# Kernel tuning notes

Hardware: AMD Instinct MI355X
Metric: run time of the kernel (lower is better)

The kernel has to match this reference:

```python
import jax, jax.numpy as jnp
import numpy as np

DIM = 1024
N_HEADS = 16
HEAD_DIM = DIM // N_HEADS
B, T = 2, 2048


def setup_inputs() -> dict:
    key = jax.random.key(0)
    ks = jax.random.split(key, 5)
    x = jax.random.normal(ks[0], (B, T, DIM), dtype=jnp.float32)
    s = DIM ** -0.5
    Wq = jax.random.normal(ks[1], (DIM, DIM), dtype=jnp.float32) * s
    Wk = jax.random.normal(ks[2], (DIM, DIM), dtype=jnp.float32) * s
    Wv = jax.random.normal(ks[3], (DIM, DIM), dtype=jnp.float32) * s
    Wo = jax.random.normal(ks[4], (DIM, DIM), dtype=jnp.float32) * s
    # causal mask: 1 where attendable, 0 where masked (masked_fill on mask==0)
    mask = jnp.tril(jnp.ones((T, T), dtype=jnp.int32))[None, None, :, :]
    return {"x": x, "Wq": Wq, "Wk": Wk, "Wv": Wv, "Wo": Wo, "mask": mask}


def _rope_tables(seq_len, dim, dtype):
    inv_freq = 1.0 / (10000.0 ** (jnp.arange(0, dim, 2, dtype=jnp.float32) / dim))
    t = jnp.arange(seq_len, dtype=jnp.float32)
    freqs = jnp.outer(t, inv_freq)               # [T, dim/2]
    emb = jnp.concatenate([freqs, freqs], -1)    # [T, dim]
    return jnp.cos(emb).astype(dtype), jnp.sin(emb).astype(dtype)


def _rotate_half(t):
    h = t.shape[-1] // 2
    return jnp.concatenate([-t[..., h:], t[..., :h]], axis=-1)


def reference(x, Wq, Wk, Wv, Wo, mask):
    Bq, Tq, C = x.shape
    H, Dh = N_HEADS, C // N_HEADS
    q = (x @ Wq.T).reshape(Bq, Tq, H, Dh)
    k = (x @ Wk.T).reshape(Bq, Tq, H, Dh)
    v = (x @ Wv.T).reshape(Bq, Tq, H, Dh)
    cos, sin = _rope_tables(Tq, Dh, x.dtype)
    cos = cos[None, :, None, :]   # [1,T,1,Dh]
    sin = sin[None, :, None, :]
    q = q * cos + _rotate_half(q) * sin
    k = k * cos + _rotate_half(k) * sin
    scale = Dh ** -0.5
    # [B,H,T,T]
    attn = jnp.einsum('bqhd,bkhd->bhqk', q, k) * scale
    attn = jnp.where(mask == 0, jnp.float32(-jnp.inf).astype(attn.dtype), attn)
    attn = jax.nn.softmax(attn, axis=-1)
    out = jnp.einsum('bhqk,bkhd->bqhd', attn, v).reshape(Bq, Tq, C)
    return out @ Wo.T
```

## Files before the change

### kernel.cpp

```cpp
#include <hip/hip_runtime.h>
#include <stdint.h>


typedef float  f32x4  __attribute__((ext_vector_type(4)));
typedef float  f32x16 __attribute__((ext_vector_type(16)));
typedef __bf16 bf16x8 __attribute__((ext_vector_type(8)));
typedef unsigned int u32x2 __attribute__((ext_vector_type(2)));

#define GLDS16(gp, lp)                                                         \
  __builtin_amdgcn_global_load_lds(                                            \
      (const __attribute__((address_space(1))) void*)(gp),                     \
      (__attribute__((address_space(3))) void*)(lp), 16, 0, 0)

static __device__ __forceinline__ f32x4 zero4() {
  f32x4 z = {0.f, 0.f, 0.f, 0.f};
  return z;
}

static __device__ __forceinline__ bf16x8 cvt8(const float* __restrict__ p) {
  f32x4 u = *(const f32x4*)p;
  f32x4 v = *(const f32x4*)(p + 4);
  bf16x8 o;
#pragma unroll
  for (int j = 0; j < 4; ++j) o[j] = (__bf16)u[j];
#pragma unroll
  for (int j = 0; j < 4; ++j) o[4 + j] = (__bf16)v[j];
  return o;
}

__global__ __launch_bounds__(256) void prep(
    const float* __restrict__ x,
    const float* __restrict__ Wq, const float* __restrict__ Wk,
    const float* __restrict__ Wv, const float* __restrict__ Wo,
    __bf16* __restrict__ xb, __bf16* __restrict__ Wb)
{
  size_t g = ((size_t)blockIdx.x * 256 + threadIdx.x) * 8;
  if (g < (size_t)4194304) {
    *(bf16x8*)&xb[g] = cvt8(x + g);
  } else {
    size_t j = g - 4194304;
    int w = (int)(j >> 20);
    size_t off = j & 1048575;
    const float* src = (w == 0) ? Wq : (w == 1) ? Wk : (w == 2) ? Wv : Wo;
    *(bf16x8*)&Wb[(size_t)w * 1048576 + off] = cvt8(src + off);
  }
}

__global__ __launch_bounds__(256) void gemm_qkv(
    const __bf16* __restrict__ xb, const __bf16* __restrict__ Wb,
    __bf16* __restrict__ Qp, __bf16* __restrict__ Kp, __bf16* __restrict__ Vt)
{
  __shared__ __bf16 Smem[2 * 128 * 64];
  __bf16* As = Smem;
  __bf16* Bs = Smem + 128 * 64;

  const int tid  = threadIdx.x;
  const int lane = tid & 63;
  const int wid  = tid >> 6;
  const int quad = lane >> 4;
  const int l16  = lane & 15;
  const int wm   = (wid >> 1) * 64;
  const int wn   = (wid & 1) * 64;

  const int lin = blockIdx.x;
  const int n0  = (lin & 7) * 128;
  const int r2  = lin >> 3;
  const int z   = r2 % 3;
  const int m0  = (r2 / 3) * 128;
  const __bf16* Bt = Wb + (size_t)z * 1048576;

  const int sr  = tid >> 3;
  const int scx = ((tid & 7) ^ (sr & 7)) * 8;
  const int fx  = l16 & 7;

  f32x4 acc[4][4];
  for (int i = 0; i < 4; ++i)
    for (int j = 0; j < 4; ++j) acc[i][j] = zero4();

  for (int k0 = 0; k0 < 1024; k0 += 64) {
    __syncthreads();
#pragma unroll
    for (int c = 0; c < 4; ++c) {
      GLDS16(xb + (size_t)(m0 + c * 32 + sr) * 1024 + k0 + scx,
             &As[c * 2048 + (size_t)tid * 8]);
      GLDS16(Bt + (size_t)(n0 + c * 32 + sr) * 1024 + k0 + scx,
             &Bs[c * 2048 + (size_t)tid * 8]);
    }
    __syncthreads();

#pragma unroll
    for (int ks = 0; ks < 2; ++ks) {
      bf16x8 af[4], bfr[4];
#pragma unroll
      for (int i = 0; i < 4; ++i)
        af[i] = *(const bf16x8*)
            &As[(wm + i * 16 + l16) * 64 + ((ks * 4 + quad) ^ fx) * 8];
#pragma unroll
      for (int i = 0; i < 4; ++i)
        bfr[i] = *(const bf16x8*)
            &Bs[(wn + i * 16 + l16) * 64 + ((ks * 4 + quad) ^ fx) * 8];
#pragma unroll
      for (int mt = 0; mt < 4; ++mt)
#pragma unroll
        for (int nt = 0; nt < 4; ++nt)
          acc[mt][nt] = __builtin_amdgcn_mfma_f32_16x16x32_bf16(
              af[mt], bfr[nt], acc[mt][nt], 0, 0, 0);
    }
  }

  __syncthreads();

  const int h = (n0 + wn) >> 6;
  __bf16* es = &Smem[wid * 1152];
  const int rl = lane >> 3, ch = lane & 7;

  if (z < 2) {
    const float c0f = -13.287712379549449f / 32.0f;
    const float f0 = exp2f((float)l16 * c0f);
    const float f1 = exp2f((float)(16 + l16) * c0f);
    const float SC = (z == 0) ? 0.125f * 1.44269504088896340736f : 1.0f;
    for (int mt = 0; mt < 4; ++mt)
      for (int r = 0; r < 4; ++r) {
        int gm = m0 + wm + mt * 16 + 4 * quad + r;
        float tt = (float)(gm & 2047);
        for (int nt = 0; nt < 2; ++nt) {
          float ang = tt * (nt ? f1 : f0);
          float cv = __cosf(ang) * SC, sv = __sinf(ang) * SC;
          float lo = acc[mt][nt][r], hi = acc[mt][nt + 2][r];
          acc[mt][nt][r]     = lo * cv - hi * sv;
          acc[mt][nt + 2][r] = hi * cv + lo * sv;
        }
      }
    __bf16* dst = (z == 0) ? Qp : Kp;
    for (int mt = 0; mt < 4; ++mt) {
      for (int nt = 0; nt < 4; ++nt)
        for (int r = 0; r < 4; ++r)
          es[(4 * quad + r) * 72 + nt * 16 + l16] = (__bf16)acc[mt][nt][r];
      size_t g0 = (size_t)(m0 + wm + mt * 16 + rl) * 1024 + n0 + wn + ch * 8;
      *(bf16x8*)&dst[g0]            = *(const bf16x8*)&es[rl * 72 + ch * 8];
      *(bf16x8*)&dst[g0 + 8 * 1024] = *(const bf16x8*)&es[(rl + 8) * 72 + ch * 8];
    }
  } else {
    const int b = m0 >> 11;
    const size_t hb = (size_t)(b * 16 + h) * 64;
    const int tt = (m0 + wm) & 2047;
    for (int nt = 0; nt < 4; ++nt) {
      for (int mt = 0; mt < 4; ++mt)
        for (int r = 0; r < 4; ++r)
          es[l16 * 72 + mt * 16 + 4 * quad + r] = (__bf16)acc[mt][nt][r];
      size_t g0 = (hb + nt * 16 + rl) * 2048 + tt + ch * 8;
      *(bf16x8*)&Vt[g0]                     = *(const bf16x8*)&es[rl * 72 + ch * 8];
      *(bf16x8*)&Vt[g0 + (size_t)8 * 2048]  = *(const bf16x8*)&es[(rl + 8) * 72 + ch * 8];
    }
  }
}

__global__ __launch_bounds__(256) void attn_fwd(
    __bf16* QA, const __bf16* __restrict__ Kp,
    const __bf16* __restrict__ Vt)
{
  __shared__ __bf16 Ks[2][64 * 64];
  __shared__ __bf16 Vs[2][64 * 64];

  const int tid  = threadIdx.x;
  const int lane = tid & 63, wid = tid >> 6;
  const int hl = lane >> 5, lq = lane & 31, lq7 = lq & 7;
  const int qh = wid & 1, kh = wid >> 1;

  const int L  = blockIdx.x;
  const int j  = L >> 3;
  const int qb = 31 - (j >> 2);
  const int bh = (L & 7) * 4 + (j & 3);
  const int b = bh >> 4, h = bh & 15;
  const int q0 = qb * 64;

  const size_t rowb = (size_t)b * 2048;
  const __bf16* Vb = Vt + (size_t)bh * 64 * 2048;

  const int srow = lane >> 3;
  const int scol = ((lane & 7) ^ srow) * 8;
  const int ck0 = wid * 2, ck1 = wid * 2 + 1;

  const int iql = qh * 32 + lq;

  bf16x8 qa[4];
#pragma unroll
  for (int ks = 0; ks < 4; ++ks)
    qa[ks] = *(const bf16x8*)
        &QA[(rowb + q0 + iql) * 1024 + h * 64 + ks * 16 + hl * 8];

  f32x16 oacc[2];
#pragma unroll
  for (int dt = 0; dt < 2; ++dt)
#pragma unroll
    for (int r = 0; r < 16; ++r) oacc[dt][r] = 0.f;
  float l_i = 0.f;

  const int kcmax = qb;

  GLDS16(Kp + (rowb + ck0 * 8 + srow) * 1024 + h * 64 + scol, &Ks[0][ck0 * 512]);
  GLDS16(Kp + (rowb + ck1 * 8 + srow) * 1024 + h * 64 + scol, &Ks[0][ck1 * 512]);
  GLDS16(Vb + (size_t)(ck0 * 8 + srow) * 2048 + scol, &Vs[0][ck0 * 512]);
  GLDS16(Vb + (size_t)(ck1 * 8 + srow) * 2048 + scol, &Vs[0][ck1 * 512]);
  __syncthreads();

  for (int kc = 0; kc <= kcmax; ++kc) {
    const int c = kc & 1;
    if (kc < kcmax) {
      const int t0 = (kc + 1) * 64;
      GLDS16(Kp + (rowb + t0 + ck0 * 8 + srow) * 1024 + h * 64 + scol,
             &Ks[c ^ 1][ck0 * 512]);
      GLDS16(Kp + (rowb + t0 + ck1 * 8 + srow) * 1024 + h * 64 + scol,
             &Ks[c ^ 1][ck1 * 512]);
      GLDS16(Vb + (size_t)(ck0 * 8 + srow) * 2048 + t0 + scol,
             &Vs[c ^ 1][ck0 * 512]);
      GLDS16(Vb + (size_t)(ck1 * 8 + srow) * 2048 + t0 + scol,
             &Vs[c ^ 1][ck1 * 512]);
    }

    const __bf16* Ksb = Ks[c];
    const __bf16* Vsb = Vs[c];

    f32x16 sacc;
#pragma unroll
    for (int r = 0; r < 16; ++r) sacc[r] = -16.f;
    __builtin_amdgcn_s_setprio(1);
#pragma unroll
    for (int ks = 0; ks < 4; ++ks) {
      bf16x8 kf = *(const bf16x8*)
          &Ksb[(kh * 32 + lq) * 64 + (((2 * ks + hl) ^ lq7) * 8)];
      sacc = __builtin_amdgcn_mfma_f32_32x32x16_bf16(kf, qa[ks], sacc, 0, 0, 0);
    }
    __builtin_amdgcn_s_setprio(0);

    const bool diag = (kc == kcmax);
    float p[16];
    float rsum = 0.f;
#pragma unroll
    for (int r = 0; r < 16; ++r) {
      float s = sacc[r];
      if (diag) {
        int kp = kh * 32 + (r & 3) + 8 * (r >> 2) + 4 * hl;
        if (kp > iql) s = -1e30f;
      }
      p[r] = __builtin_amdgcn_exp2f(s);
      rsum += p[r];
    }
    rsum += __shfl_xor(rsum, 32, 64);
    l_i += rsum;

    unsigned int cpk[8];
#pragma unroll
    for (int i = 0; i < 8; ++i)
      asm("v_cvt_pk_bf16_f32 %0, %1, %2"
          : "=v"(cpk[i]) : "v"(p[2 * i]), "v"(p[2 * i + 1]));
    bf16x8 pb[2];
#pragma unroll
    for (int k2 = 0; k2 < 2; ++k2) {
      unsigned int a0 = cpk[4 * k2 + 0], b0 = cpk[4 * k2 + 2];
      unsigned int a1 = cpk[4 * k2 + 1], b1 = cpk[4 * k2 + 3];
      asm("v_permlane32_swap_b32 %0, %1" : "+v"(a0), "+v"(b0));
      asm("v_permlane32_swap_b32 %0, %1" : "+v"(a1), "+v"(b1));
      union { unsigned int w[4]; bf16x8 v; } u;
      u.w[0] = a0; u.w[1] = a1; u.w[2] = b0; u.w[3] = b1;
      pb[k2] = u.v;
    }

    __builtin_amdgcn_s_setprio(1);
#pragma unroll
    for (int dt = 0; dt < 2; ++dt)
#pragma unroll
      for (int k2 = 0; k2 < 2; ++k2) {
        bf16x8 vf = *(const bf16x8*)
            &Vsb[(dt * 32 + lq) * 64 + (((4 * kh + 2 * k2 + hl) ^ lq7) * 8)];
        oacc[dt] = __builtin_amdgcn_mfma_f32_32x32x16_bf16(
            vf, pb[k2], oacc[dt], 0, 0, 0);
      }
    __builtin_amdgcn_s_setprio(0);

    __syncthreads();
  }

  float* Osf = (float*)&Ks[0][0];
  float* Lsf = (float*)&Vs[0][0];
  if (kh == 1) {
#pragma unroll
    for (int dt = 0; dt < 2; ++dt) {
      float* base = &Osf[((qh * 2 + dt) * 64 + lane) * 16];
#pragma unroll
      for (int g = 0; g < 4; ++g) {
        f32x4 w = {oacc[dt][4 * g], oacc[dt][4 * g + 1],
                   oacc[dt][4 * g + 2], oacc[dt][4 * g + 3]};
        *(f32x4*)&base[4 * g] = w;
      }
    }
    Lsf[qh * 64 + lane] = l_i;
  }
  __syncthreads();
  if (kh == 0) {
#pragma unroll
    for (int dt = 0; dt < 2; ++dt) {
      const float* base = &Osf[((qh * 2 + dt) * 64 + lane) * 16];
#pragma unroll
      for (int g = 0; g < 4; ++g) {
        f32x4 w = *(const f32x4*)&base[4 * g];
#pragma unroll
        for (int e = 0; e < 4; ++e) oacc[dt][4 * g + e] += w[e];
      }
    }
    float inv = 1.0f / (l_i + Lsf[qh * 64 + lane]);
#pragma unroll
    for (int dt = 0; dt < 2; ++dt)
#pragma unroll
      for (int g = 0; g < 4; ++g) {
        float a = oacc[dt][4 * g]     * inv, bb = oacc[dt][4 * g + 1] * inv;
        float cc = oacc[dt][4 * g + 2] * inv, dd = oacc[dt][4 * g + 3] * inv;
        unsigned int w0, w1;
        asm("v_cvt_pk_bf16_f32 %0, %1, %2" : "=v"(w0) : "v"(a), "v"(bb));
        asm("v_cvt_pk_bf16_f32 %0, %1, %2" : "=v"(w1) : "v"(cc), "v"(dd));
        u32x2 wv = {w0, w1};
        *(u32x2*)&QA[(rowb + q0 + iql) * 1024 + h * 64 + dt * 32 + 8 * g + 4 * hl] = wv;
      }
  }
}

__global__ __launch_bounds__(256) void gemm_out(
    const __bf16* __restrict__ AO, const __bf16* __restrict__ Wob,
    float* __restrict__ Of)
{
  __shared__ __bf16 Smem[2 * 128 * 64];
  __bf16* As = Smem;
  __bf16* Bs = Smem + 128 * 64;

  const int tid  = threadIdx.x;
  const int lane = tid & 63;
  const int wid  = tid >> 6;
  const int quad = lane >> 4;
  const int l16  = lane & 15;
  const int wm   = (wid >> 1) * 64;
  const int wn   = (wid & 1) * 64;

  const int lin = blockIdx.x;
  const int n0  = (lin & 7) * 128;
  const int m0  = (lin >> 3) * 128;

  const int sr  = tid >> 3;
  const int scx = ((tid & 7) ^ (sr & 7)) * 8;
  const int fx  = l16 & 7;

  f32x4 acc[4][4];
  for (int i = 0; i < 4; ++i)
    for (int j = 0; j < 4; ++j) acc[i][j] = zero4();

  for (int k0 = 0; k0 < 1024; k0 += 64) {
    __syncthreads();
#pragma unroll
    for (int c = 0; c < 4; ++c) {
      GLDS16(AO  + (size_t)(m0 + c * 32 + sr) * 1024 + k0 + scx,
             &As[c * 2048 + (size_t)tid * 8]);
      GLDS16(Wob + (size_t)(n0 + c * 32 + sr) * 1024 + k0 + scx,
             &Bs[c * 2048 + (size_t)tid * 8]);
    }
    __syncthreads();

#pragma unroll
    for (int ks = 0; ks < 2; ++ks) {
      bf16x8 af[4], bfr[4];
#pragma unroll
      for (int i = 0; i < 4; ++i)
        af[i] = *(const bf16x8*)
            &As[(wm + i * 16 + l16) * 64 + ((ks * 4 + quad) ^ fx) * 8];
#pragma unroll
      for (int i = 0; i < 4; ++i)
        bfr[i] = *(const bf16x8*)
            &Bs[(wn + i * 16 + l16) * 64 + ((ks * 4 + quad) ^ fx) * 8];
#pragma unroll
      for (int mt = 0; mt < 4; ++mt)
#pragma unroll
        for (int nt = 0; nt < 4; ++nt)
          acc[mt][nt] = __builtin_amdgcn_mfma_f32_16x16x32_bf16(
              af[mt], bfr[nt], acc[mt][nt], 0, 0, 0);
    }
  }

  __syncthreads();

  float* es = (float*)&Smem[0] + wid * 1088;
  const int rl = lane >> 4, ch = lane & 15;
  for (int mt = 0; mt < 4; ++mt) {
    for (int nt = 0; nt < 4; ++nt)
      for (int r = 0; r < 4; ++r)
        es[(4 * quad + r) * 68 + nt * 16 + l16] = acc[mt][nt][r];
    size_t g0 = (size_t)(m0 + wm + mt * 16 + rl) * 1024 + n0 + wn + ch * 4;
    *(f32x4*)&Of[g0]             = *(const f32x4*)&es[rl * 68 + ch * 4];
    *(f32x4*)&Of[g0 + 4 * 1024]  = *(const f32x4*)&es[(rl + 4) * 68 + ch * 4];
    *(f32x4*)&Of[g0 + 8 * 1024]  = *(const f32x4*)&es[(rl + 8) * 68 + ch * 4];
    *(f32x4*)&Of[g0 + 12 * 1024] = *(const f32x4*)&es[(rl + 12) * 68 + ch * 4];
  }
}

__global__ __launch_bounds__(256) void copy_bf16x8(
    const __bf16* __restrict__ src, __bf16* __restrict__ dst)
{
  size_t i = ((size_t)blockIdx.x * 256 + threadIdx.x) * 8;
  *(bf16x8*)&dst[i] = *(const bf16x8*)&src[i];
}

extern "C" void kernel_launch(void* const* d_in, const int* in_sizes, int n_in,
                              void* d_out, int out_size, void* d_ws, size_t ws_size,
                              hipStream_t stream) {
  const float* x  = (const float*)d_in[0];
  const float* Wq = (const float*)d_in[1];
  const float* Wk = (const float*)d_in[2];
  const float* Wv = (const float*)d_in[3];
  const float* Wo = (const float*)d_in[4];
  float* out = (float*)d_out;

  const size_t NELT = (size_t)4194304;
  __bf16* Qp = (__bf16*)d_ws;
  __bf16* Kp = Qp + NELT;
  __bf16* Vt = Kp + NELT;
  __bf16* xb = (__bf16*)d_out;
  __bf16* Wb = xb + NELT;

  prep<<<dim3(4096), 256, 0, stream>>>(x, Wq, Wk, Wv, Wo, xb, Wb);
  gemm_qkv<<<dim3(768), 256, 0, stream>>>(xb, Wb, Qp, Kp, Vt);
  attn_fwd<<<dim3(1024), 256, 0, stream>>>(Qp, Kp, Vt);
  copy_bf16x8<<<dim3(512), 256, 0, stream>>>(Wb + 3 * NELT / 4, Kp);
  gemm_out<<<dim3(256), 256, 0, stream>>>(Qp, Kp, out);
}
```

Before: 194.7 us.

## Shrink GEMM K-tile to 32 and halve out-projection M-tile for more blocks

Both GEMMs now stage 32-wide K slices instead of 64, with a matching 4-column XOR swizzle, which halves LDS use per block and may raise occupancy. The output projection also moves to 64x128 tiles, doubling the grid from 256 to 512 blocks so more CUs are busy on a 4096x1024 problem. In exchange there are twice as many K iterations and barriers per block, and the epilogue now syncs after each row tile because the staging buffer overlaps across waves.

```diff
diff --git a/kernel.cpp b/kernel.cpp
--- a/kernel.cpp
+++ b/kernel.cpp
@@ -50,9 +50,9 @@
     const __bf16* __restrict__ xb, const __bf16* __restrict__ Wb,
     __bf16* __restrict__ Qp, __bf16* __restrict__ Kp, __bf16* __restrict__ Vt)
 {
-  __shared__ __bf16 Smem[2 * 128 * 64];
+  __shared__ __bf16 Smem[2 * 128 * 32];
   __bf16* As = Smem;
-  __bf16* Bs = Smem + 128 * 64;
+  __bf16* Bs = Smem + 128 * 32;
 
   const int tid  = threadIdx.x;
   const int lane = tid & 63;
@@ -69,43 +69,38 @@
   const int m0  = (r2 / 3) * 128;
   const __bf16* Bt = Wb + (size_t)z * 1048576;
 
-  const int sr  = tid >> 3;
-  const int scx = ((tid & 7) ^ (sr & 7)) * 8;
-  const int fx  = l16 & 7;
+  const int r0 = tid >> 2, c0 = tid & 3;
+  const int r1 = r0 + 64;
+  const int scx = (c0 ^ ((r0 >> 1) & 3)) * 8;
+  const int fq  = (l16 >> 1) & 3;
 
   f32x4 acc[4][4];
   for (int i = 0; i < 4; ++i)
     for (int j = 0; j < 4; ++j) acc[i][j] = zero4();
 
-  for (int k0 = 0; k0 < 1024; k0 += 64) {
-    __syncthreads();
-#pragma unroll
-    for (int c = 0; c < 4; ++c) {
-      GLDS16(xb + (size_t)(m0 + c * 32 + sr) * 1024 + k0 + scx,
-             &As[c * 2048 + (size_t)tid * 8]);
-      GLDS16(Bt + (size_t)(n0 + c * 32 + sr) * 1024 + k0 + scx,
-             &Bs[c * 2048 + (size_t)tid * 8]);
-    }
-    __syncthreads();
-
-#pragma unroll
-    for (int ks = 0; ks < 2; ++ks) {
-      bf16x8 af[4], bfr[4];
-#pragma unroll
-      for (int i = 0; i < 4; ++i)
-        af[i] = *(const bf16x8*)
-            &As[(wm + i * 16 + l16) * 64 + ((ks * 4 + quad) ^ fx) * 8];
-#pragma unroll
-      for (int i = 0; i < 4; ++i)
-        bfr[i] = *(const bf16x8*)
-            &Bs[(wn + i * 16 + l16) * 64 + ((ks * 4 + quad) ^ fx) * 8];
-#pragma unroll
-      for (int mt = 0; mt < 4; ++mt)
-#pragma unroll
-        for (int nt = 0; nt < 4; ++nt)
-          acc[mt][nt] = __builtin_amdgcn_mfma_f32_16x16x32_bf16(
-              af[mt], bfr[nt], acc[mt][nt], 0, 0, 0);
-    }
+  for (int k0 = 0; k0 < 1024; k0 += 32) {
+    __syncthreads();
+    GLDS16(xb + (size_t)(m0 + r0) * 1024 + k0 + scx, &As[(size_t)tid * 8]);
+    GLDS16(xb + (size_t)(m0 + r1) * 1024 + k0 + scx, &As[(size_t)(tid + 256) * 8]);
+    GLDS16(Bt + (size_t)(n0 + r0) * 1024 + k0 + scx, &Bs[(size_t)tid * 8]);
+    GLDS16(Bt + (size_t)(n0 + r1) * 1024 + k0 + scx, &Bs[(size_t)(tid + 256) * 8]);
+    __syncthreads();
+
+    bf16x8 af[4], bfr[4];
+#pragma unroll
+    for (int i = 0; i < 4; ++i)
+      af[i] = *(const bf16x8*)
+          &As[(wm + i * 16 + l16) * 32 + ((quad ^ fq) * 8)];
+#pragma unroll
+    for (int i = 0; i < 4; ++i)
+      bfr[i] = *(const bf16x8*)
+          &Bs[(wn + i * 16 + l16) * 32 + ((quad ^ fq) * 8)];
+#pragma unroll
+    for (int mt = 0; mt < 4; ++mt)
+#pragma unroll
+      for (int nt = 0; nt < 4; ++nt)
+        acc[mt][nt] = __builtin_amdgcn_mfma_f32_16x16x32_bf16(
+            af[mt], bfr[nt], acc[mt][nt], 0, 0, 0);
   }
 
   __syncthreads();
@@ -328,66 +323,60 @@
     const __bf16* __restrict__ AO, const __bf16* __restrict__ Wob,
     float* __restrict__ Of)
 {
-  __shared__ __bf16 Smem[2 * 128 * 64];
+  __shared__ __bf16 Smem[8704];
   __bf16* As = Smem;
-  __bf16* Bs = Smem + 128 * 64;
+  __bf16* Bs = Smem + 64 * 32;
 
   const int tid  = threadIdx.x;
   const int lane = tid & 63;
   const int wid  = tid >> 6;
   const int quad = lane >> 4;
   const int l16  = lane & 15;
-  const int wm   = (wid >> 1) * 64;
+  const int wm   = (wid >> 1) * 32;
   const int wn   = (wid & 1) * 64;
 
   const int lin = blockIdx.x;
   const int n0  = (lin & 7) * 128;
-  const int m0  = (lin >> 3) * 128;
-
-  const int sr  = tid >> 3;
-  const int scx = ((tid & 7) ^ (sr & 7)) * 8;
-  const int fx  = l16 & 7;
-
-  f32x4 acc[4][4];
-  for (int i = 0; i < 4; ++i)
+  const int m0  = (lin >> 3) * 64;
+
+  const int r0 = tid >> 2, c0 = tid & 3;
+  const int scx = (c0 ^ ((r0 >> 1) & 3)) * 8;
+  const int fq  = (l16 >> 1) & 3;
+
+  f32x4 acc[2][4];
+  for (int i = 0; i < 2; ++i)
     for (int j = 0; j < 4; ++j) acc[i][j] = zero4();
 
-  for (int k0 = 0; k0 < 1024; k0 += 64) {
-    __syncthreads();
-#pragma unroll
-    for (int c = 0; c < 4; ++c) {
-      GLDS16(AO  + (size_t)(m0 + c * 32 + sr) * 1024 + k0 + scx,
-             &As[c * 2048 + (size_t)tid * 8]);
-      GLDS16(Wob + (size_t)(n0 + c * 32 + sr) * 1024 + k0 + scx,
-             &Bs[c * 2048 + (size_t)tid * 8]);
-    }
-    __syncthreads();
-
-#pragma unroll
-    for (int ks = 0; ks < 2; ++ks) {
-      bf16x8 af[4], bfr[4];
-#pragma unroll
-      for (int i = 0; i < 4; ++i)
-        af[i] = *(const bf16x8*)
-            &As[(wm + i * 16 + l16) * 64 + ((ks * 4 + quad) ^ fx) * 8];
-#pragma unroll
-      for (int i = 0; i < 4; ++i)
-        bfr[i] = *(const bf16x8*)
-            &Bs[(wn + i * 16 + l16) * 64 + ((ks * 4 + quad) ^ fx) * 8];
-#pragma unroll
-      for (int mt = 0; mt < 4; ++mt)
-#pragma unroll
-        for (int nt = 0; nt < 4; ++nt)
-          acc[mt][nt] = __builtin_amdgcn_mfma_f32_16x16x32_bf16(
-              af[mt], bfr[nt], acc[mt][nt], 0, 0, 0);
-    }
+  for (int k0 = 0; k0 < 1024; k0 += 32) {
+    __syncthreads();
+    GLDS16(AO  + (size_t)(m0 + r0) * 1024 + k0 + scx, &As[(size_t)tid * 8]);
+    GLDS16(Wob + (size_t)(n0 + r0) * 1024 + k0 + scx, &Bs[(size_t)tid * 8]);
+    GLDS16(Wob + (size_t)(n0 + 64 + r0) * 1024 + k0 + scx,
+           &Bs[(size_t)(tid + 256) * 8]);
+    __syncthreads();
+
+    bf16x8 af[2], bfr[4];
+#pragma unroll
+    for (int i = 0; i < 2; ++i)
+      af[i] = *(const bf16x8*)
+          &As[(wm + i * 16 + l16) * 32 + ((quad ^ fq) * 8)];
+#pragma unroll
+    for (int i = 0; i < 4; ++i)
+      bfr[i] = *(const bf16x8*)
+          &Bs[(wn + i * 16 + l16) * 32 + ((quad ^ fq) * 8)];
+#pragma unroll
+    for (int mt = 0; mt < 2; ++mt)
+#pragma unroll
+      for (int nt = 0; nt < 4; ++nt)
+        acc[mt][nt] = __builtin_amdgcn_mfma_f32_16x16x32_bf16(
+            af[mt], bfr[nt], acc[mt][nt], 0, 0, 0);
   }
 
   __syncthreads();
 
   float* es = (float*)&Smem[0] + wid * 1088;
   const int rl = lane >> 4, ch = lane & 15;
-  for (int mt = 0; mt < 4; ++mt) {
+  for (int mt = 0; mt < 2; ++mt) {
     for (int nt = 0; nt < 4; ++nt)
       for (int r = 0; r < 4; ++r)
         es[(4 * quad + r) * 68 + nt * 16 + l16] = acc[mt][nt][r];
@@ -396,6 +385,7 @@
     *(f32x4*)&Of[g0 + 4 * 1024]  = *(const f32x4*)&es[(rl + 4) * 68 + ch * 4];
     *(f32x4*)&Of[g0 + 8 * 1024]  = *(const f32x4*)&es[(rl + 8) * 68 + ch * 4];
     *(f32x4*)&Of[g0 + 12 * 1024] = *(const f32x4*)&es[(rl + 12) * 68 + ch * 4];
+    __syncthreads();
   }
 }
 
@@ -427,5 +417,5 @@
   gemm_qkv<<<dim3(768), 256, 0, stream>>>(xb, Wb, Qp, Kp, Vt);
   attn_fwd<<<dim3(1024), 256, 0, stream>>>(Qp, Kp, Vt);
   copy_bf16x8<<<dim3(512), 256, 0, stream>>>(Wb + 3 * NELT / 4, Kp);
-  gemm_out<<<dim3(256), 256, 0, stream>>>(Qp, Kp, out);
-}
+  gemm_out<<<dim3(512), 256, 0, stream>>>(Qp, Kp, out);
+}
```

New measurement: 184.7 us. -5.1%, faster.
